# Kernel tuning notes

Hardware: AMD Instinct MI355X
Metric: run time of the kernel (lower is better)

## Reference

```python
import jax, jax.numpy as jnp
import numpy as np

H, W, L = 512, 512, 28
N_ITER = 12
SIGMA = 0.5
LAM = 1.0
PI = 3.141592653589793


def _offsets(s, phi_deg):
    # Matches torch: dx = s*cos(phi), dy = s*sin(phi), shifted to min 0, round-half-even.
    phi = phi_deg * PI / 180.0
    dx = s * np.cos(phi)
    dy = s * np.sin(phi)
    dx = dx - dx.min()
    dy = dy - dy.min()
    return np.rint(dx).astype(np.int32), np.rint(dy).astype(np.int32)


def _gauss_kernel(sigma):
    ksize = max(3, int(6 * sigma + 1) | 1)  # 5 for sigma=0.5
    ax = np.arange(ksize, dtype=np.float32) - ksize // 2
    g1 = np.exp(-0.5 * (ax / sigma) ** 2)
    g1 = g1 / g1.sum()
    g2 = np.outer(g1, g1).astype(np.float32)
    return jnp.asarray(g2)[None, None], ksize // 2  # [1,1,k,k], pad


def setup_inputs():
    k1, k2 = jax.random.split(jax.random.key(0))
    s_nom = jnp.arange(L, dtype=jnp.float32)
    phi_d_deg = jnp.ones((), dtype=jnp.float32)
    dx, dy = _offsets(np.arange(L, dtype=np.float32), 1.0)
    Hp, Wp = H + int(dy.max()), W + int(dx.max())
    y_1hw = jax.random.uniform(k1, (1, Hp, Wp), dtype=jnp.float32)
    mask2d = jax.random.uniform(k2, (H, W), dtype=jnp.float32)
    return {"y_1hw": y_1hw, "mask2d": mask2d, "phi_d_deg": phi_d_deg, "s_nom": s_nom}


def reference(y_1hw, mask2d, phi_d_deg, s_nom):
    # Integer dispersion offsets are detached (.item()) in the original, so they
    # are compile-time constants here.
    dx, dy = _offsets(np.asarray(s_nom), float(np.asarray(phi_d_deg)))
    Hp, Wp = H + int(dy.max()), W + int(dx.max())
    rows = dy[:, None, None] + np.arange(H, dtype=np.int64)[None, :, None]  # [L,H,1]
    cols = dx[:, None, None] + np.arange(W, dtype=np.int64)[None, None, :]  # [L,1,W]
    flat = jnp.asarray(rows * Wp + cols)  # [L,H,W] flat indices into [Hp*Wp]

    g2, pad = _gauss_kernel(SIGMA)

    def A(x):  # CASSI forward: [L,H,W] -> [Hp,Wp] batched scatter-add
        return jnp.zeros(Hp * Wp, x.dtype).at[flat].add(mask2d[None] * x).reshape(Hp, Wp)

    def At(y2):  # CASSI adjoint: [Hp,Wp] -> [L,H,W] batched gather
        return y2.reshape(-1)[flat] * mask2d[None]

    def denoise(x):  # depthwise 5x5 Gaussian; same 2D kernel per band -> bands as batch
        return jax.lax.conv_general_dilated(
            x[:, None], g2, (1, 1), [(pad, pad), (pad, pad)])[:, 0]

    # Phi_sum = sum over bands of shifted mask, clamped to >= 1
    Phi_sum = jnp.maximum(
        jnp.zeros(Hp * Wp, mask2d.dtype).at[flat].add(
            jnp.broadcast_to(mask2d[None], (L, H, W))).reshape(Hp, Wp),
        1.0)

    y = y_1hw[0]
    x = At(y)   # adjoint back-projection initialization
    y1 = y
    for _ in range(N_ITER):  # unrolled GAP iterations (accelerated GAP)
        yb = A(x)
        y1 = y1 + (y - yb)
        x = x + LAM * At((y1 - yb) / Phi_sum)
        x = denoise(x)
    return x[None]  # [1, L, H, W]
```

## Files before the change

### kernel.cpp

```cpp
#include <hip/hip_runtime.h>

#define HH 512
#define WW 512
#define LL 28
#define WP 539
#define NPIX (HH * WP)
#define NX (LL * HH * WW)

#define TX 64
#define TY 16
#define GB 7
#define NGRP (LL / GB)

__global__ void k_setup(const float* __restrict__ y, const float* __restrict__ mask,
                        float* __restrict__ phi_inv, float* __restrict__ y1) {
    int idx = blockIdx.x * blockDim.x + threadIdx.x;
    if (idx >= NPIX) return;
    int i = idx / WP, jp = idx - i * WP;
    int lmin = jp - (WW - 1); if (lmin < 0) lmin = 0;
    int lmax = jp < (LL - 1) ? jp : (LL - 1);
    float s = 0.f;
    for (int l = lmin; l <= lmax; ++l) s += mask[i * WW + (jp - l)];
    phi_inv[idx] = 1.0f / fmaxf(s, 1.0f);
    y1[idx] = y[idx];
}

__global__ __launch_bounds__(256) void k_xinit(const float* __restrict__ y, const float* __restrict__ mask,
                        float* __restrict__ x, float* __restrict__ yb) {
    __shared__ float ybl[TY][TX + GB - 1];
    const int l0 = blockIdx.z * GB;
    const int bi = blockIdx.y * TY;
    const int bj = blockIdx.x * TX;
    const int tid = threadIdx.x;
    const int tx = tid & 63;
    const int ty = tid >> 6;

    #pragma unroll
    for (int k = 0; k < 4; ++k) {
        int r = ty + 4 * k;
        ybl[r][tx] = 0.f;
        if (tx < GB - 1) ybl[r][64 + tx] = 0.f;
    }
    __syncthreads();

    for (int l = l0; l < l0 + GB; ++l) {
        #pragma unroll
        for (int k = 0; k < 4; ++k) {
            int r = ty + 4 * k;
            int gi = bi + r, gj = bj + tx;
            float m = mask[gi * WW + gj];
            float v = y[gi * WP + gj + l] * m;
            x[((size_t)l * HH + gi) * WW + gj] = v;
            ybl[r][tx + (l - l0)] += m * v;
        }
        __syncthreads();
    }
    #pragma unroll
    for (int k = 0; k < 4; ++k) {
        int r = ty + 4 * k;
        atomicAdd(&yb[(bi + r) * WP + bj + l0 + tx], ybl[r][tx]);
        if (tx < GB - 1) atomicAdd(&yb[(bi + r) * WP + bj + l0 + 64 + tx], ybl[r][64 + tx]);
    }
}

__global__ __launch_bounds__(256) void k_pix(const float* __restrict__ y, const float* __restrict__ phi_inv,
                      float* __restrict__ y1, float* __restrict__ t, float* __restrict__ yb) {
    int idx = blockIdx.x * blockDim.x + threadIdx.x;
    if (idx >= NPIX / 4) return;
    float4 ybv = ((const float4*)yb)[idx];
    float4 yv  = ((const float4*)y)[idx];
    float4 y1v = ((const float4*)y1)[idx];
    float4 pv  = ((const float4*)phi_inv)[idx];
    float4 y1n, tv;
    y1n.x = y1v.x + yv.x - ybv.x;  tv.x = (y1n.x - ybv.x) * pv.x;
    y1n.y = y1v.y + yv.y - ybv.y;  tv.y = (y1n.y - ybv.y) * pv.y;
    y1n.z = y1v.z + yv.z - ybv.z;  tv.z = (y1n.z - ybv.z) * pv.z;
    y1n.w = y1v.w + yv.w - ybv.w;  tv.w = (y1n.w - ybv.w) * pv.w;
    ((float4*)y1)[idx] = y1n;
    ((float4*)t)[idx]  = tv;
    ((float4*)yb)[idx] = make_float4(0.f, 0.f, 0.f, 0.f);
}

template <bool LAST>
__global__ __launch_bounds__(256) void k_iter(const float* __restrict__ x, const float* __restrict__ t,
                       const float* __restrict__ mask, float* __restrict__ xo,
                       float* __restrict__ yb, float w0, float w1, float w2) {
    __shared__ float msk[TY + 4][TX + 4];
    __shared__ float tld[TY + 4][TX + 4 + GB - 1];
    __shared__ float u[TY + 4][TX + 4];
    __shared__ float hb[TY + 4][TX];
    __shared__ float ybl[TY][TX + GB - 1];

    const int l0 = blockIdx.z * GB;
    const int bi = blockIdx.y * TY;
    const int bj = blockIdx.x * TX;
    const int tid = threadIdx.x;
    const int tx = tid & 63;
    const int ty = tid >> 6;
    const bool edge = (bi == 0) | (bi == HH - TY) | (bj == 0) | (bj == WW - TX);

    #pragma unroll
    for (int k = 0; k < 5; ++k) {
        int r = ty + 4 * k;
        int gi = bi + r - 2;
        bool rok = (gi >= 0) & (gi < HH);
        int gj0 = bj + tx - 2;
        float m0 = 0.f;
        if (rok & (gj0 >= 0) & (gj0 < WW)) m0 = mask[gi * WW + gj0];
        msk[r][tx] = m0;
        if (tx < 4) {
            int gj1 = bj + 64 + tx - 2;
            float m1 = 0.f;
            if (rok & (gj1 < WW)) m1 = mask[gi * WW + gj1];
            msk[r][64 + tx] = m1;
        }
        int tg0 = bj - 2 + l0 + tx;
        float v0 = 0.f;
        if (rok & (tg0 >= 0) & (tg0 < WP)) v0 = t[gi * WP + tg0];
        tld[r][tx] = v0;
        if (tx < 4 + GB - 1) {
            int tg1 = tg0 + 64;
            float v1 = 0.f;
            if (rok & (tg1 < WP)) v1 = t[gi * WP + tg1];
            tld[r][64 + tx] = v1;
        }
    }
    if (!LAST) {
        #pragma unroll
        for (int k = 0; k < 4; ++k) {
            int r = ty + 4 * k;
            ybl[r][tx] = 0.f;
            if (tx < GB - 1) ybl[r][64 + tx] = 0.f;
        }
    }
    __syncthreads();

    for (int l = l0; l < l0 + GB; ++l) {
        const float* xl = x + (size_t)l * HH * WW;
        const int dl = l - l0;
        if (!edge) {
            #pragma unroll
            for (int k = 0; k < 5; ++k) {
                int r = ty + 4 * k;
                const float* xrow = xl + (bi + r - 2) * WW + bj - 2;
                u[r][tx] = fmaf(tld[r][tx + dl], msk[r][tx], xrow[tx]);
                if (tx < 4) u[r][64 + tx] = fmaf(tld[r][64 + tx + dl], msk[r][64 + tx], xrow[64 + tx]);
            }
        } else {
            #pragma unroll
            for (int k = 0; k < 5; ++k) {
                int r = ty + 4 * k;
                int gi = bi + r - 2;
                bool rok = (gi >= 0) & (gi < HH);
                int gj0 = bj + tx - 2;
                float v0 = 0.f;
                if (rok & (gj0 >= 0) & (gj0 < WW))
                    v0 = fmaf(tld[r][tx + dl], msk[r][tx], xl[gi * WW + gj0]);
                u[r][tx] = v0;
                if (tx < 4) {
                    int gj1 = bj + 64 + tx - 2;
                    float v1 = 0.f;
                    if (rok & (gj1 < WW))
                        v1 = fmaf(tld[r][64 + tx + dl], msk[r][64 + tx], xl[gi * WW + gj1]);
                    u[r][64 + tx] = v1;
                }
            }
        }
        __syncthreads();
        #pragma unroll
        for (int k = 0; k < 5; ++k) {
            int r = ty + 4 * k;
            hb[r][tx] = w2 * (u[r][tx] + u[r][tx + 4])
                      + w1 * (u[r][tx + 1] + u[r][tx + 3])
                      + w0 * u[r][tx + 2];
        }
        __syncthreads();
        #pragma unroll
        for (int k = 0; k < 4; ++k) {
            int r = ty + 4 * k;
            float o = w2 * (hb[r][tx] + hb[r + 4][tx])
                    + w1 * (hb[r + 1][tx] + hb[r + 3][tx])
                    + w0 * hb[r + 2][tx];
            xo[((size_t)l * HH + bi + r) * WW + bj + tx] = o;
            if (!LAST) ybl[r][tx + dl] += msk[r + 2][tx + 2] * o;
        }
        __syncthreads();
    }

    if (!LAST) {
        #pragma unroll
        for (int k = 0; k < 4; ++k) {
            int r = ty + 4 * k;
            atomicAdd(&yb[(bi + r) * WP + bj + l0 + tx], ybl[r][tx]);
            if (tx < GB - 1) atomicAdd(&yb[(bi + r) * WP + bj + l0 + 64 + tx], ybl[r][64 + tx]);
        }
    }
}

extern "C" void kernel_launch(void* const* d_in, const int* in_sizes, int n_in,
                              void* d_out, int out_size, void* d_ws, size_t ws_size,
                              hipStream_t stream) {
    const float* y    = (const float*)d_in[0];
    const float* mask = (const float*)d_in[1];

    float* out = (float*)d_out;

    float* phi_inv = (float*)d_ws;
    float* y1      = phi_inv + NPIX;
    float* t       = y1 + NPIX;
    float* yb      = t + NPIX;
    float* xA      = yb + NPIX;
    float* xB      = out;

    float g1 = expf(-2.0f), g2 = expf(-8.0f);
    float gs = 1.0f + 2.0f * g1 + 2.0f * g2;
    float w0 = 1.0f / gs, w1 = g1 / gs, w2 = g2 / gs;

    const int BT = 256;
    const dim3 tgrid(WW / TX, HH / TY, NGRP);

    hipMemsetAsync(yb, 0, NPIX * sizeof(float), stream);
    k_setup<<<(NPIX + BT - 1) / BT, BT, 0, stream>>>(y, mask, phi_inv, y1);
    k_xinit<<<tgrid, BT, 0, stream>>>(y, mask, xB, yb);

    float* cur = xB;
    float* nxt = xA;
    for (int it = 0; it < 12; ++it) {
        k_pix<<<(NPIX / 4 + BT - 1) / BT, BT, 0, stream>>>(y, phi_inv, y1, t, yb);
        if (it < 11)
            k_iter<false><<<tgrid, BT, 0, stream>>>(cur, t, mask, nxt, yb, w0, w1, w2);
        else
            k_iter<true><<<tgrid, BT, 0, stream>>>(cur, t, mask, nxt, yb, w0, w1, w2);
        float* tmp = cur; cur = nxt; nxt = tmp;
    }
}
```

Before: 550.1 us.

## Fuse GAP iterations into a persistent cooperative megakernel with grid syncs

Replaces the setup, init, per-pixel and per-iteration kernel launches with one cooperative persistent kernel. Iterations are separated by grid-wide syncs, and tiles are walked by a grid-stride loop. The per-pixel y1/t update is folded into each tile's halo load, and a triple-buffered yb lets the zeroing and accumulation happen in the same phase, so one grid sync per iteration is enough. The initial A(At(y)) is computed directly as y times the sum of squared mask values, which skips the atomics in the init kernel. In exchange, every tile now recomputes t for its halo, the interior fast path without bounds checks is gone, and correctness depends on grid-sync cost and cooperative-launch occupancy.

```diff
diff --git a/kernel.cpp b/kernel.cpp
--- a/kernel.cpp
+++ b/kernel.cpp
@@ -1,4 +1,7 @@
 #include <hip/hip_runtime.h>
+#include <hip/hip_cooperative_groups.h>
+
+namespace cg = cooperative_groups;
 
 #define HH 512
 #define WW 512
@@ -10,190 +13,182 @@
 #define TX 64
 #define TY 16
 #define GB 7
-#define NGRP (LL / GB)
-
-__global__ void k_setup(const float* __restrict__ y, const float* __restrict__ mask,
-                        float* __restrict__ phi_inv, float* __restrict__ y1) {
-    int idx = blockIdx.x * blockDim.x + threadIdx.x;
-    if (idx >= NPIX) return;
-    int i = idx / WP, jp = idx - i * WP;
-    int lmin = jp - (WW - 1); if (lmin < 0) lmin = 0;
-    int lmax = jp < (LL - 1) ? jp : (LL - 1);
-    float s = 0.f;
-    for (int l = lmin; l <= lmax; ++l) s += mask[i * WW + (jp - l)];
-    phi_inv[idx] = 1.0f / fmaxf(s, 1.0f);
-    y1[idx] = y[idx];
-}
-
-__global__ __launch_bounds__(256) void k_xinit(const float* __restrict__ y, const float* __restrict__ mask,
-                        float* __restrict__ x, float* __restrict__ yb) {
-    __shared__ float ybl[TY][TX + GB - 1];
-    const int l0 = blockIdx.z * GB;
-    const int bi = blockIdx.y * TY;
-    const int bj = blockIdx.x * TX;
+#define NTILE (8 * 32 * 4)
+
+__global__ __launch_bounds__(256, 4) void k_mega(
+    const float* __restrict__ y, const float* __restrict__ mask,
+    float* __restrict__ xOut,
+    float* __restrict__ xWs,
+    float* __restrict__ phi_inv,
+    float* __restrict__ y1U, float* __restrict__ y1V,
+    float* __restrict__ ybP, float* __restrict__ ybQ, float* __restrict__ ybR,
+    float w0, float w1, float w2)
+{
+    cg::grid_group grid = cg::this_grid();
     const int tid = threadIdx.x;
     const int tx = tid & 63;
     const int ty = tid >> 6;
-
-    #pragma unroll
-    for (int k = 0; k < 4; ++k) {
-        int r = ty + 4 * k;
-        ybl[r][tx] = 0.f;
-        if (tx < GB - 1) ybl[r][64 + tx] = 0.f;
-    }
-    __syncthreads();
-
-    for (int l = l0; l < l0 + GB; ++l) {
-        #pragma unroll
-        for (int k = 0; k < 4; ++k) {
-            int r = ty + 4 * k;
-            int gi = bi + r, gj = bj + tx;
-            float m = mask[gi * WW + gj];
-            float v = y[gi * WP + gj + l] * m;
-            x[((size_t)l * HH + gi) * WW + gj] = v;
-            ybl[r][tx + (l - l0)] += m * v;
-        }
-        __syncthreads();
-    }
-    #pragma unroll
-    for (int k = 0; k < 4; ++k) {
-        int r = ty + 4 * k;
-        atomicAdd(&yb[(bi + r) * WP + bj + l0 + tx], ybl[r][tx]);
-        if (tx < GB - 1) atomicAdd(&yb[(bi + r) * WP + bj + l0 + 64 + tx], ybl[r][64 + tx]);
-    }
-}
-
-__global__ __launch_bounds__(256) void k_pix(const float* __restrict__ y, const float* __restrict__ phi_inv,
-                      float* __restrict__ y1, float* __restrict__ t, float* __restrict__ yb) {
-    int idx = blockIdx.x * blockDim.x + threadIdx.x;
-    if (idx >= NPIX / 4) return;
-    float4 ybv = ((const float4*)yb)[idx];
-    float4 yv  = ((const float4*)y)[idx];
-    float4 y1v = ((const float4*)y1)[idx];
-    float4 pv  = ((const float4*)phi_inv)[idx];
-    float4 y1n, tv;
-    y1n.x = y1v.x + yv.x - ybv.x;  tv.x = (y1n.x - ybv.x) * pv.x;
-    y1n.y = y1v.y + yv.y - ybv.y;  tv.y = (y1n.y - ybv.y) * pv.y;
-    y1n.z = y1v.z + yv.z - ybv.z;  tv.z = (y1n.z - ybv.z) * pv.z;
-    y1n.w = y1v.w + yv.w - ybv.w;  tv.w = (y1n.w - ybv.w) * pv.w;
-    ((float4*)y1)[idx] = y1n;
-    ((float4*)t)[idx]  = tv;
-    ((float4*)yb)[idx] = make_float4(0.f, 0.f, 0.f, 0.f);
-}
-
-template <bool LAST>
-__global__ __launch_bounds__(256) void k_iter(const float* __restrict__ x, const float* __restrict__ t,
-                       const float* __restrict__ mask, float* __restrict__ xo,
-                       float* __restrict__ yb, float w0, float w1, float w2) {
+    const int nblk = gridDim.x;
+    const int gthreads = nblk * 256;
+    const int gtid = blockIdx.x * 256 + tid;
+
     __shared__ float msk[TY + 4][TX + 4];
     __shared__ float tld[TY + 4][TX + 4 + GB - 1];
     __shared__ float u[TY + 4][TX + 4];
     __shared__ float hb[TY + 4][TX];
     __shared__ float ybl[TY][TX + GB - 1];
 
-    const int l0 = blockIdx.z * GB;
-    const int bi = blockIdx.y * TY;
-    const int bj = blockIdx.x * TX;
-    const int tid = threadIdx.x;
-    const int tx = tid & 63;
-    const int ty = tid >> 6;
-    const bool edge = (bi == 0) | (bi == HH - TY) | (bj == 0) | (bj == WW - TX);
-
-    #pragma unroll
-    for (int k = 0; k < 5; ++k) {
-        int r = ty + 4 * k;
-        int gi = bi + r - 2;
-        bool rok = (gi >= 0) & (gi < HH);
-        int gj0 = bj + tx - 2;
-        float m0 = 0.f;
-        if (rok & (gj0 >= 0) & (gj0 < WW)) m0 = mask[gi * WW + gj0];
-        msk[r][tx] = m0;
-        if (tx < 4) {
-            int gj1 = bj + 64 + tx - 2;
-            float m1 = 0.f;
-            if (rok & (gj1 < WW)) m1 = mask[gi * WW + gj1];
-            msk[r][64 + tx] = m1;
+    for (int idx = gtid; idx < NPIX; idx += gthreads) {
+        int i = idx / WP, jp = idx - i * WP;
+        int lmin = jp - (WW - 1); if (lmin < 0) lmin = 0;
+        int lmax = jp < (LL - 1) ? jp : (LL - 1);
+        float s = 0.f, sq = 0.f;
+        for (int l = lmin; l <= lmax; ++l) {
+            float m = mask[i * WW + (jp - l)];
+            s += m; sq = fmaf(m, m, sq);
         }
-        int tg0 = bj - 2 + l0 + tx;
-        float v0 = 0.f;
-        if (rok & (tg0 >= 0) & (tg0 < WP)) v0 = t[gi * WP + tg0];
-        tld[r][tx] = v0;
-        if (tx < 4 + GB - 1) {
-            int tg1 = tg0 + 64;
-            float v1 = 0.f;
-            if (rok & (tg1 < WP)) v1 = t[gi * WP + tg1];
-            tld[r][64 + tx] = v1;
+        phi_inv[idx] = 1.0f / fmaxf(s, 1.0f);
+        float yv = y[idx];
+        y1U[idx] = yv;
+        ybP[idx] = yv * sq;
+        ybQ[idx] = 0.f;
+    }
+    for (int idx = gtid; idx < NX; idx += gthreads) {
+        int l = idx / (HH * WW);
+        int r = idx - l * HH * WW;
+        int i = r >> 9, j = r & 511;
+        xOut[idx] = y[i * WP + j + l] * mask[r];
+    }
+    grid.sync();
+
+    float* xcur = xOut;
+    float* xnxt = xWs;
+    float* ybbuf[3] = {ybP, ybQ, ybR};
+
+    for (int it = 0; it < 12; ++it) {
+        const float* ybRd = ybbuf[it % 3];
+        float* ybAc = ybbuf[(it + 1) % 3];
+        float* ybZe = ybbuf[(it + 2) % 3];
+        const float* y1in = (it & 1) ? y1V : y1U;
+        float* y1out      = (it & 1) ? y1U : y1V;
+        const bool last = (it == 11);
+
+        if (!last) {
+            for (int idx = gtid; idx < NPIX; idx += gthreads) {
+                float yb_ = ybRd[idx];
+                y1out[idx] = y1in[idx] + y[idx] - yb_;
+                ybZe[idx] = 0.f;
+            }
         }
-    }
-    if (!LAST) {
-        #pragma unroll
-        for (int k = 0; k < 4; ++k) {
-            int r = ty + 4 * k;
-            ybl[r][tx] = 0.f;
-            if (tx < GB - 1) ybl[r][64 + tx] = 0.f;
-        }
-    }
-    __syncthreads();
-
-    for (int l = l0; l < l0 + GB; ++l) {
-        const float* xl = x + (size_t)l * HH * WW;
-        const int dl = l - l0;
-        if (!edge) {
-            #pragma unroll
-            for (int k = 0; k < 5; ++k) {
-                int r = ty + 4 * k;
-                const float* xrow = xl + (bi + r - 2) * WW + bj - 2;
-                u[r][tx] = fmaf(tld[r][tx + dl], msk[r][tx], xrow[tx]);
-                if (tx < 4) u[r][64 + tx] = fmaf(tld[r][64 + tx + dl], msk[r][64 + tx], xrow[64 + tx]);
-            }
-        } else {
+
+        for (int tt = blockIdx.x; tt < NTILE; tt += nblk) {
+            const int bj = (tt & 7) * TX;
+            const int bi = ((tt >> 3) & 31) * TY;
+            const int l0 = (tt >> 8) * GB;
+
+            __syncthreads();
+
             #pragma unroll
             for (int k = 0; k < 5; ++k) {
                 int r = ty + 4 * k;
                 int gi = bi + r - 2;
                 bool rok = (gi >= 0) & (gi < HH);
                 int gj0 = bj + tx - 2;
-                float v0 = 0.f;
-                if (rok & (gj0 >= 0) & (gj0 < WW))
-                    v0 = fmaf(tld[r][tx + dl], msk[r][tx], xl[gi * WW + gj0]);
-                u[r][tx] = v0;
+                float m0 = 0.f;
+                if (rok & (gj0 >= 0) & (gj0 < WW)) m0 = mask[gi * WW + gj0];
+                msk[r][tx] = m0;
                 if (tx < 4) {
                     int gj1 = bj + 64 + tx - 2;
+                    float m1 = 0.f;
+                    if (rok & (gj1 < WW)) m1 = mask[gi * WW + gj1];
+                    msk[r][64 + tx] = m1;
+                }
+                int tg0 = bj + l0 - 2 + tx;
+                float v0 = 0.f;
+                if (rok & (tg0 >= 0) & (tg0 < WP)) {
+                    int p = gi * WP + tg0;
+                    float yb_ = ybRd[p];
+                    float y1n = y1in[p] + y[p] - yb_;
+                    v0 = (y1n - yb_) * phi_inv[p];
+                }
+                tld[r][tx] = v0;
+                if (tx < 4 + GB - 1) {
+                    int tg1 = tg0 + 64;
                     float v1 = 0.f;
-                    if (rok & (gj1 < WW))
-                        v1 = fmaf(tld[r][64 + tx + dl], msk[r][64 + tx], xl[gi * WW + gj1]);
-                    u[r][64 + tx] = v1;
+                    if (rok & (tg1 >= 0) & (tg1 < WP)) {
+                        int p = gi * WP + tg1;
+                        float yb_ = ybRd[p];
+                        float y1n = y1in[p] + y[p] - yb_;
+                        v1 = (y1n - yb_) * phi_inv[p];
+                    }
+                    tld[r][64 + tx] = v1;
+                }
+            }
+            if (!last) {
+                #pragma unroll
+                for (int k = 0; k < 4; ++k) {
+                    int r = ty + 4 * k;
+                    ybl[r][tx] = 0.f;
+                    if (tx < GB - 1) ybl[r][64 + tx] = 0.f;
+                }
+            }
+            __syncthreads();
+
+            for (int l = l0; l < l0 + GB; ++l) {
+                const float* xl = xcur + (size_t)l * HH * WW;
+                const int dl = l - l0;
+                #pragma unroll
+                for (int k = 0; k < 5; ++k) {
+                    int r = ty + 4 * k;
+                    int gi = bi + r - 2;
+                    bool rok = (gi >= 0) & (gi < HH);
+                    int gj0 = bj + tx - 2;
+                    float v0 = 0.f;
+                    if (rok & (gj0 >= 0) & (gj0 < WW))
+                        v0 = fmaf(tld[r][tx + dl], msk[r][tx], xl[gi * WW + gj0]);
+                    u[r][tx] = v0;
+                    if (tx < 4) {
+                        int gj1 = bj + 64 + tx - 2;
+                        float v1 = 0.f;
+                        if (rok & (gj1 < WW))
+                            v1 = fmaf(tld[r][64 + tx + dl], msk[r][64 + tx], xl[gi * WW + gj1]);
+                        u[r][64 + tx] = v1;
+                    }
+                }
+                __syncthreads();
+                #pragma unroll
+                for (int k = 0; k < 5; ++k) {
+                    int r = ty + 4 * k;
+                    hb[r][tx] = w2 * (u[r][tx] + u[r][tx + 4])
+                              + w1 * (u[r][tx + 1] + u[r][tx + 3])
+                              + w0 * u[r][tx + 2];
+                }
+                __syncthreads();
+                #pragma unroll
+                for (int k = 0; k < 4; ++k) {
+                    int r = ty + 4 * k;
+                    float o = w2 * (hb[r][tx] + hb[r + 4][tx])
+                            + w1 * (hb[r + 1][tx] + hb[r + 3][tx])
+                            + w0 * hb[r + 2][tx];
+                    xnxt[((size_t)l * HH + bi + r) * WW + bj + tx] = o;
+                    if (!last) ybl[r][tx + dl] += msk[r + 2][tx + 2] * o;
+                }
+                __syncthreads();
+            }
+
+            if (!last) {
+                #pragma unroll
+                for (int k = 0; k < 4; ++k) {
+                    int r = ty + 4 * k;
+                    atomicAdd(&ybAc[(bi + r) * WP + bj + l0 + tx], ybl[r][tx]);
+                    if (tx < GB - 1)
+                        atomicAdd(&ybAc[(bi + r) * WP + bj + l0 + 64 + tx], ybl[r][64 + tx]);
                 }
             }
         }
-        __syncthreads();
-        #pragma unroll
-        for (int k = 0; k < 5; ++k) {
-            int r = ty + 4 * k;
-            hb[r][tx] = w2 * (u[r][tx] + u[r][tx + 4])
-                      + w1 * (u[r][tx + 1] + u[r][tx + 3])
-                      + w0 * u[r][tx + 2];
-        }
-        __syncthreads();
-        #pragma unroll
-        for (int k = 0; k < 4; ++k) {
-            int r = ty + 4 * k;
-            float o = w2 * (hb[r][tx] + hb[r + 4][tx])
-                    + w1 * (hb[r + 1][tx] + hb[r + 3][tx])
-                    + w0 * hb[r + 2][tx];
-            xo[((size_t)l * HH + bi + r) * WW + bj + tx] = o;
-            if (!LAST) ybl[r][tx + dl] += msk[r + 2][tx + 2] * o;
-        }
-        __syncthreads();
-    }
-
-    if (!LAST) {
-        #pragma unroll
-        for (int k = 0; k < 4; ++k) {
-            int r = ty + 4 * k;
-            atomicAdd(&yb[(bi + r) * WP + bj + l0 + tx], ybl[r][tx]);
-            if (tx < GB - 1) atomicAdd(&yb[(bi + r) * WP + bj + l0 + 64 + tx], ybl[r][64 + tx]);
-        }
+
+        grid.sync();
+        float* tmp = xcur; xcur = xnxt; xnxt = tmp;
     }
 }
 
@@ -203,34 +198,32 @@
     const float* y    = (const float*)d_in[0];
     const float* mask = (const float*)d_in[1];
 
-    float* out = (float*)d_out;
+    float* xOut = (float*)d_out;
 
     float* phi_inv = (float*)d_ws;
-    float* y1      = phi_inv + NPIX;
-    float* t       = y1 + NPIX;
-    float* yb      = t + NPIX;
-    float* xA      = yb + NPIX;
-    float* xB      = out;
+    float* y1U     = phi_inv + NPIX;
+    float* y1V     = y1U + NPIX;
+    float* ybP     = y1V + NPIX;
+    float* ybQ     = ybP + NPIX;
+    float* ybR     = ybQ + NPIX;
+    float* xWs     = ybR + NPIX;
 
     float g1 = expf(-2.0f), g2 = expf(-8.0f);
     float gs = 1.0f + 2.0f * g1 + 2.0f * g2;
     float w0 = 1.0f / gs, w1 = g1 / gs, w2 = g2 / gs;
 
-    const int BT = 256;
-    const dim3 tgrid(WW / TX, HH / TY, NGRP);
-
-    hipMemsetAsync(yb, 0, NPIX * sizeof(float), stream);
-    k_setup<<<(NPIX + BT - 1) / BT, BT, 0, stream>>>(y, mask, phi_inv, y1);
-    k_xinit<<<tgrid, BT, 0, stream>>>(y, mask, xB, yb);
-
-    float* cur = xB;
-    float* nxt = xA;
-    for (int it = 0; it < 12; ++it) {
-        k_pix<<<(NPIX / 4 + BT - 1) / BT, BT, 0, stream>>>(y, phi_inv, y1, t, yb);
-        if (it < 11)
-            k_iter<false><<<tgrid, BT, 0, stream>>>(cur, t, mask, nxt, yb, w0, w1, w2);
-        else
-            k_iter<true><<<tgrid, BT, 0, stream>>>(cur, t, mask, nxt, yb, w0, w1, w2);
-        float* tmp = cur; cur = nxt; nxt = tmp;
-    }
+    int nCU = 256;
+    hipDeviceGetAttribute(&nCU, hipDeviceAttributeMultiprocessorCount, 0);
+    int perCU = 0;
+    hipOccupancyMaxActiveBlocksPerMultiprocessor(&perCU, k_mega, 256, 0);
+    int blocks = perCU * nCU;
+    if (blocks > 1024) blocks = 1024;
+    if (blocks < 256) blocks = 256;
+
+    void* args[] = {(void*)&y, (void*)&mask, (void*)&xOut, (void*)&xWs,
+                    (void*)&phi_inv, (void*)&y1U, (void*)&y1V,
+                    (void*)&ybP, (void*)&ybQ, (void*)&ybR,
+                    (void*)&w0, (void*)&w1, (void*)&w2};
+    hipLaunchCooperativeKernel((const void*)k_mega, dim3(blocks), dim3(256),
+                               args, 0, stream);
 }
```

New measurement: 1.962 ms. +256.7%, slower.
